# Kernel tuning notes

Measured on AMD Instinct MI355X. Metric: run time of the kernel, lower is better.

## Reference

```python
import jax, jax.numpy as jnp
import numpy as np

BS, S, D, H, DFF, L = 8, 1024, 256, 8, 1024, 3
DK = D // H
NEG = -1e32


def setup_inputs() -> dict:
    key = jax.random.key(0)
    ks = jax.random.split(key, 10)
    r = lambda k, shp: jax.random.normal(k, shp, jnp.float32) * 0.02
    return {
        "q_embed_data": jax.random.normal(ks[0], (BS, S, D), jnp.float32),
        "qa_embed_data": jax.random.normal(ks[1], (BS, S, D), jnp.float32),
        "Wk": r(ks[2], (L, D, D)), "bk": jnp.zeros((L, D), jnp.float32),
        "Wv": r(ks[3], (L, D, D)), "bv": jnp.zeros((L, D), jnp.float32),
        "Wo": r(ks[4], (L, D, D)), "bo": jnp.zeros((L, D), jnp.float32),
        "gammas": r(ks[5], (L, H)),
        "ln1_g": jnp.ones((L, D), jnp.float32), "ln1_b": jnp.zeros((L, D), jnp.float32),
        "W1": r(ks[6], (L, D, DFF)), "b1": jnp.zeros((L, DFF), jnp.float32),
        "W2": r(ks[7], (L, DFF, D)), "b2": jnp.zeros((L, D), jnp.float32),
        "ln2_g": jnp.ones((L, D), jnp.float32), "ln2_b": jnp.zeros((L, D), jnp.float32),
    }


def _layernorm(x, g, b, eps=1e-5):
    mu = x.mean(-1, keepdims=True)
    var = ((x - mu) ** 2).mean(-1, keepdims=True)
    return (x - mu) * jax.lax.rsqrt(var + eps) * g + b


def _attn(xq, xk, xv, Wk, bk, Wv, bv, Wo, bo, gamma, mask, zero_pad):
    # kq_same=1: q and k both use k_linear
    bs = xq.shape[0]
    q = (xq @ Wk + bk).reshape(bs, S, H, DK).transpose(0, 2, 1, 3)  # bhsd
    k = (xk @ Wk + bk).reshape(bs, S, H, DK).transpose(0, 2, 1, 3)
    v = (xv @ Wv + bv).reshape(bs, S, H, DK).transpose(0, 2, 1, 3)
    scores = jnp.einsum('bhid,bhjd->bhij', q, k) / np.float32(np.sqrt(DK))
    mf = mask.astype(scores.dtype)
    # no-grad decay branch (detached in torch)
    p = jax.nn.softmax(jnp.where(mask, scores, NEG), axis=-1) * mf
    distcum = jnp.cumsum(p, axis=-1)
    disttot = p.sum(axis=-1, keepdims=True)
    idx = jnp.arange(S)
    pos = jnp.abs(idx[None, :] - idx[:, None]).astype(jnp.float32)[None, None]
    dist = jnp.sqrt(jnp.clip((disttot - distcum) * pos, 0.0, None))
    dist = jax.lax.stop_gradient(dist)
    g = -jax.nn.softplus(gamma)[None, :, None, None]  # (1,H,1,1)
    total_effect = jnp.clip(jnp.exp(dist * g), 1e-5, 1e5)
    scores = scores * total_effect
    attn = jax.nn.softmax(jnp.where(mask, scores, NEG), axis=-1)
    if zero_pad:
        attn = attn.at[:, :, 0, :].set(0.0)
    out = jnp.einsum('bhij,bhjd->bhid', attn, v)
    out = out.transpose(0, 2, 1, 3).reshape(bs, S, D)
    return out @ Wo + bo


def _block(i, xq, xk, xv, mask, zero_pad, apply_pos, P):
    Wk, bk, Wv, bv, Wo, bo, gam, l1g, l1b, W1, b1, W2, b2, l2g, l2b = [p[i] for p in P]
    q2 = _attn(xq, xk, xv, Wk, bk, Wv, bv, Wo, bo, gam, mask, zero_pad)
    x = _layernorm(xq + q2, l1g, l1b)
    if apply_pos:
        ff = jax.nn.relu(x @ W1 + b1) @ W2 + b2
        x = _layernorm(x + ff, l2g, l2b)
    return x


def _forward(q_embed_data, qa_embed_data, Wk, bk, Wv, bv, Wo, bo, gammas,
             ln1_g, ln1_b, W1, b1, W2, b2, ln2_g, ln2_b):
    P = (Wk, bk, Wv, bv, Wo, bo, gammas, ln1_g, ln1_b, W1, b1, W2, b2, ln2_g, ln2_b)
    tri_incl = jnp.tril(jnp.ones((S, S), bool))[None, None]       # mask=1: peek current+past
    tri_excl = jnp.tril(jnp.ones((S, S), bool), -1)[None, None]   # mask=0: strictly past
    x, y = q_embed_data, qa_embed_data
    # blocks_1 (n_blocks=1): mask=1, apply_pos=True, self-attn on y
    y = _block(0, y, y, y, tri_incl, False, True, P)
    # blocks_2 (2*n_blocks=2): alternate (mask=1, no FFN) / (mask=0, zero_pad, FFN, values=y)
    x = _block(1, x, x, x, tri_incl, False, False, P)
    x = _block(2, x, x, y, tri_excl, True, True, P)
    return x


def reference(q_embed_data, qa_embed_data, Wk, bk, Wv, bv, Wo, bo, gammas,
              ln1_g, ln1_b, W1, b1, W2, b2, ln2_g, ln2_b):
    return _forward(q_embed_data, qa_embed_data, Wk, bk, Wv, bv, Wo, bo, gammas,
                    ln1_g, ln1_b, W1, b1, W2, b2, ln2_g, ln2_b)
```

## Files before the change

kernel.cpp:

```cpp
#include <hip/hip_runtime.h>

typedef unsigned short u16;
typedef float f32x4 __attribute__((ext_vector_type(4)));
typedef __bf16 bf16x8 __attribute__((ext_vector_type(8)));
typedef u16 u16x8 __attribute__((ext_vector_type(8)));
typedef u16 u16x4 __attribute__((ext_vector_type(4)));

__device__ __forceinline__ u16 f2bf(float f) {
  union { float f; unsigned u; } v; v.f = f;
  unsigned r = (v.u + 0x7FFFu + ((v.u >> 16) & 1u)) >> 16;
  return (u16)r;
}
__device__ __forceinline__ unsigned pack2bf(float a, float b) {
  return (unsigned)f2bf(a) | ((unsigned)f2bf(b) << 16);
}
__device__ __forceinline__ float wred_sum(float v) {
#pragma unroll
  for (int o = 32; o >= 1; o >>= 1) v += __shfl_xor(v, o);
  return v;
}

template <int RELU, int WF32, int WBF, int WVT>
__global__ __launch_bounds__(256) void gemm_kernel(
    const u16* __restrict__ A, const u16* __restrict__ Bt,
    const float* __restrict__ bias, float* __restrict__ C,
    u16* __restrict__ Cbf, int M, int N, int K) {
  __shared__ u16 As[64 * 64];
  __shared__ u16 Bs[64 * 64];
  const int tid = threadIdx.x;
  const int lane = tid & 63;
  const int w = tid >> 6;
  const int m0 = blockIdx.x * 64;
  const int n0 = blockIdx.y * 64;
  const int wr = (w >> 1) * 32;
  const int wc = (w & 1) * 32;
  const int l15 = lane & 15, hi = lane >> 4;

  f32x4 acc[2][2] = {};

  for (int k0 = 0; k0 < K; k0 += 64) {
#pragma unroll
    for (int rep = 0; rep < 2; ++rep) {
      int idx = tid + rep * 256;
      int row = idx >> 3, c8 = idx & 7;
      int cs = ((c8 ^ (row & 7)) << 3);
      __builtin_amdgcn_global_load_lds(
          (const __attribute__((address_space(1))) void*)(A + (size_t)(m0 + row) * K + k0 + cs),
          (__attribute__((address_space(3))) void*)(&As[idx * 8]), 16, 0, 0);
      __builtin_amdgcn_global_load_lds(
          (const __attribute__((address_space(1))) void*)(Bt + (size_t)(n0 + row) * K + k0 + cs),
          (__attribute__((address_space(3))) void*)(&Bs[idx * 8]), 16, 0, 0);
    }
    __syncthreads();
#pragma unroll
    for (int kk = 0; kk < 2; ++kk) {
      int kb = (kk * 32 + (hi << 3)) << 1;
      bf16x8 af[2], bfr[2];
#pragma unroll
      for (int mf = 0; mf < 2; ++mf) {
        int m = wr + mf * 16 + l15;
        af[mf] = *(const bf16x8*)((const char*)As + m * 128 + (kb ^ ((m & 7) << 4)));
      }
#pragma unroll
      for (int nf = 0; nf < 2; ++nf) {
        int n = wc + nf * 16 + l15;
        bfr[nf] = *(const bf16x8*)((const char*)Bs + n * 128 + (kb ^ ((n & 7) << 4)));
      }
#pragma unroll
      for (int mf = 0; mf < 2; ++mf)
#pragma unroll
        for (int nf = 0; nf < 2; ++nf)
          acc[mf][nf] = __builtin_amdgcn_mfma_f32_16x16x32_bf16(af[mf], bfr[nf], acc[mf][nf], 0, 0, 0);
    }
    __syncthreads();
  }

#pragma unroll
  for (int mf = 0; mf < 2; ++mf)
#pragma unroll
    for (int nf = 0; nf < 2; ++nf) {
      int col = n0 + wc + nf * 16 + l15;
      float bia = bias[col];
      u16x4 tv;
#pragma unroll
      for (int r = 0; r < 4; ++r) {
        int row = m0 + wr + mf * 16 + (hi << 2) + r;
        float val = acc[mf][nf][r] + bia;
        if (RELU) val = fmaxf(val, 0.f);
        if (WF32) C[(size_t)row * N + col] = val;
        if (WBF) Cbf[(size_t)row * N + col] = f2bf(val);
        if (WVT) tv[r] = f2bf(val);
      }
      if (WVT) {
        int row0 = m0 + wr + mf * 16 + (hi << 2);
        size_t addr = (((size_t)(row0 >> 10) * 8 + (col >> 5)) * 32 + (col & 31)) * 1024 + (row0 & 1023);
        *(u16x4*)(Cbf + addr) = tv;
      }
    }
}

__global__ __launch_bounds__(256) void gemm_kv_kernel(
    const u16* __restrict__ A, const u16* __restrict__ Bt,
    const float* __restrict__ biasK, const float* __restrict__ biasV,
    u16* __restrict__ qkbf, u16* __restrict__ vT, int M, int N, int K) {
  __shared__ u16 As[64 * 64];
  __shared__ u16 Bs[64 * 64];
  const int tid = threadIdx.x;
  const int lane = tid & 63;
  const int w = tid >> 6;
  const int m0 = blockIdx.x * 64;
  const int n0 = blockIdx.y * 64;
  const int wr = (w >> 1) * 32;
  const int wc = (w & 1) * 32;
  const int l15 = lane & 15, hi = lane >> 4;

  f32x4 acc[2][2] = {};

  for (int k0 = 0; k0 < K; k0 += 64) {
#pragma unroll
    for (int rep = 0; rep < 2; ++rep) {
      int idx = tid + rep * 256;
      int row = idx >> 3, c8 = idx & 7;
      int cs = ((c8 ^ (row & 7)) << 3);
      __builtin_amdgcn_global_load_lds(
          (const __attribute__((address_space(1))) void*)(A + (size_t)(m0 + row) * K + k0 + cs),
          (__attribute__((address_space(3))) void*)(&As[idx * 8]), 16, 0, 0);
      __builtin_amdgcn_global_load_lds(
          (const __attribute__((address_space(1))) void*)(Bt + (size_t)(n0 + row) * K + k0 + cs),
          (__attribute__((address_space(3))) void*)(&Bs[idx * 8]), 16, 0, 0);
    }
    __syncthreads();
#pragma unroll
    for (int kk = 0; kk < 2; ++kk) {
      int kb = (kk * 32 + (hi << 3)) << 1;
      bf16x8 af[2], bfr[2];
#pragma unroll
      for (int mf = 0; mf < 2; ++mf) {
        int m = wr + mf * 16 + l15;
        af[mf] = *(const bf16x8*)((const char*)As + m * 128 + (kb ^ ((m & 7) << 4)));
      }
#pragma unroll
      for (int nf = 0; nf < 2; ++nf) {
        int n = wc + nf * 16 + l15;
        bfr[nf] = *(const bf16x8*)((const char*)Bs + n * 128 + (kb ^ ((n & 7) << 4)));
      }
#pragma unroll
      for (int mf = 0; mf < 2; ++mf)
#pragma unroll
        for (int nf = 0; nf < 2; ++nf)
          acc[mf][nf] = __builtin_amdgcn_mfma_f32_16x16x32_bf16(af[mf], bfr[nf], acc[mf][nf], 0, 0, 0);
    }
    __syncthreads();
  }

  const bool isV = (n0 >= 256);
#pragma unroll
  for (int mf = 0; mf < 2; ++mf)
#pragma unroll
    for (int nf = 0; nf < 2; ++nf) {
      int col = n0 + wc + nf * 16 + l15;
      float bia = isV ? biasV[col - 256] : biasK[col];
      u16x4 tv;
#pragma unroll
      for (int r = 0; r < 4; ++r) {
        int row = m0 + wr + mf * 16 + (hi << 2) + r;
        float val = acc[mf][nf][r] + bia;
        if (!isV) qkbf[(size_t)row * 256 + col] = f2bf(val);
        tv[r] = f2bf(val);
      }
      if (isV) {
        int row0 = m0 + wr + mf * 16 + (hi << 2);
        int vc = col - 256;
        size_t addr = (((size_t)(row0 >> 10) * 8 + (vc >> 5)) * 32 + (vc & 31)) * 1024 + (row0 & 1023);
        *(u16x4*)(vT + addr) = tv;
      }
    }
}

__global__ __launch_bounds__(256) void attn_mfma_kernel(
    const u16* __restrict__ qkbf, const u16* __restrict__ vT,
    u16* __restrict__ ao, const float* __restrict__ gam, int excl) {
  __shared__ float zbuf[4][16];
  __shared__ float z2buf[4][16];
  __shared__ float accbuf[8][4][64];

  const int lane = threadIdx.x & 63, w = threadIdx.x >> 6;
  const int qt = 63 - blockIdx.y;
  const int bh = blockIdx.x;
  const int b = bh >> 3, h = bh & 7;
  const int q0 = qt * 16;
  const int l15 = lane & 15, hi = lane >> 4;
  const int i = q0 + l15;
  const float g = -log1pf(__expf(gam[h]));
  const float scale = 0.17677669529663687f;

  const u16* kbase = qkbf + ((size_t)b * 1024) * 256 + h * 32;
  const bf16x8 qfrag = *(const bf16x8*)(kbase + (size_t)(q0 + l15) * 256 + hi * 8);

  const int mylim = i - excl;
  const int jmax = q0 + 15 - excl;
  const int ntiles = (jmax >> 4) + 1;
  const int C = (ntiles + 3) >> 2;
  const int c0 = w * C;
  const int tEnd = (c0 + C < ntiles) ? (c0 + C) : ntiles;
  const int count = (tEnd > c0) ? (tEnd - c0) : 0;

  float zacc = 0.f;
  for (int t = c0; t < tEnd; ++t) {
    bf16x8 kf = *(const bf16x8*)(kbase + (size_t)(t * 16 + l15) * 256 + hi * 8);
    f32x4 sA = {};
    sA = __builtin_amdgcn_mfma_f32_16x16x32_bf16(kf, qfrag, sA, 0, 0, 0);
    const int kb = t * 16 + hi * 4;
#pragma unroll
    for (int r = 0; r < 4; ++r)
      if (kb + r <= mylim) zacc += __expf(sA[r] * scale);
  }
  zacc += __shfl_xor(zacc, 16);
  zacc += __shfl_xor(zacc, 32);
  if (lane < 16) zbuf[w][lane] = zacc;
  __syncthreads();

  const float zc0 = zbuf[0][l15], zc1 = zbuf[1][l15];
  const float zc2 = zbuf[2][l15], zc3 = zbuf[3][l15];
  const float Z = zc0 + zc1 + zc2 + zc3;
  const float invZ = Z > 0.f ? 1.f / Z : 0.f;
  float prefix = 0.f;
  if (w > 0) prefix += zc0;
  if (w > 1) prefix += zc1;
  if (w > 2) prefix += zc2;

  const u16* vbase = vT + (size_t)bh * 32 * 1024;
  float carry = prefix * invZ, z2 = 0.f;
  f32x4 accO0 = {}, accO1 = {};
  unsigned pk00 = 0, pk01 = 0;
  const int Cp = (count + 1) & ~1;
  for (int tl = 0; tl < Cp; ++tl) {
    const int t = c0 + tl;
    const bool tv = tl < count;
    float ep[4] = {0.f, 0.f, 0.f, 0.f};
    if (tv) {
      bf16x8 kf = *(const bf16x8*)(kbase + (size_t)(t * 16 + l15) * 256 + hi * 8);
      f32x4 sA = {};
      sA = __builtin_amdgcn_mfma_f32_16x16x32_bf16(kf, qfrag, sA, 0, 0, 0);
      const int kb = t * 16 + hi * 4;
      float sv[4], p[4];
#pragma unroll
      for (int r = 0; r < 4; ++r) {
        sv[r] = sA[r] * scale;
        p[r] = (kb + r <= mylim) ? __expf(sv[r]) * invZ : 0.f;
      }
      float c1 = p[0] + p[1];
      float c2 = c1 + p[2];
      float c3 = c2 + p[3];
      float vsc = c3;
      float tmp = __shfl_up(vsc, 16); if (hi >= 1) vsc += tmp;
      tmp = __shfl_up(vsc, 32); if (hi >= 2) vsc += tmp;
      const float exg = vsc - c3;
      const float tot = __shfl(vsc, l15 + 48);
      const float cb = carry + exg;
      float cum[4] = {cb + p[0], cb + c1, cb + c2, cb + c3};
      carry += tot;
#pragma unroll
      for (int r = 0; r < 4; ++r) {
        if (kb + r <= mylim) {
          float pos = (float)(i - (kb + r));
          float dist = sqrtf(fmaxf((1.f - cum[r]) * pos, 0.f));
          float te = fmaxf(__expf(dist * g), 1e-5f);
          float e = __expf(sv[r] * te);
          ep[r] = e;
          z2 += e;
        }
      }
    }
    unsigned u0 = pack2bf(ep[0], ep[1]);
    unsigned u1 = pack2bf(ep[2], ep[3]);
    if ((tl & 1) == 0) {
      pk00 = u0; pk01 = u1;
    } else {
      const int srcA = l15 + (((2 * hi) & 3) << 4);
      const int srcB = l15 + (((2 * hi + 1) & 3) << 4);
      unsigned a00 = (unsigned)__shfl((int)pk00, srcA);
      unsigned a01 = (unsigned)__shfl((int)u0,   srcA);
      unsigned a10 = (unsigned)__shfl((int)pk01, srcA);
      unsigned a11 = (unsigned)__shfl((int)u1,   srcA);
      unsigned b00 = (unsigned)__shfl((int)pk00, srcB);
      unsigned b01 = (unsigned)__shfl((int)u0,   srcB);
      unsigned b10 = (unsigned)__shfl((int)pk01, srcB);
      unsigned b11 = (unsigned)__shfl((int)u1,   srcB);
      const bool up = hi >= 2;
      union { unsigned u[4]; bf16x8 v; } pf;
      pf.u[0] = up ? a01 : a00;
      pf.u[1] = up ? a11 : a10;
      pf.u[2] = up ? b01 : b00;
      pf.u[3] = up ? b11 : b10;
      const int jb = (t - 1) * 16;
      bf16x8 vf0 = *(const bf16x8*)(vbase + (size_t)l15 * 1024 + jb + hi * 8);
      bf16x8 vf1 = *(const bf16x8*)(vbase + (size_t)(16 + l15) * 1024 + jb + hi * 8);
      accO0 = __builtin_amdgcn_mfma_f32_16x16x32_bf16(vf0, pf.v, accO0, 0, 0, 0);
      accO1 = __builtin_amdgcn_mfma_f32_16x16x32_bf16(vf1, pf.v, accO1, 0, 0, 0);
    }
  }

  z2 += __shfl_xor(z2, 16);
  z2 += __shfl_xor(z2, 32);
  if (lane < 16) z2buf[w][lane] = z2;
#pragma unroll
  for (int j = 0; j < 4; ++j) {
    accbuf[j][w][lane] = accO0[j];
    accbuf[4 + j][w][lane] = accO1[j];
  }
  __syncthreads();

  if (w == 0) {
    const float z2t = z2buf[0][l15] + z2buf[1][l15] + z2buf[2][l15] + z2buf[3][l15];
    const float inv2 = z2t > 0.f ? 1.f / z2t : 0.f;
    u16* aop = ao + ((size_t)(b * 1024 + i)) * 256 + h * 32;
    u16x4 o0, o1;
#pragma unroll
    for (int j = 0; j < 4; ++j) {
      float s0 = accbuf[j][0][lane] + accbuf[j][1][lane] + accbuf[j][2][lane] + accbuf[j][3][lane];
      float s1 = accbuf[4 + j][0][lane] + accbuf[4 + j][1][lane] + accbuf[4 + j][2][lane] + accbuf[4 + j][3][lane];
      o0[j] = f2bf(s0 * inv2);
      o1[j] = f2bf(s1 * inv2);
    }
    *(u16x4*)(aop + hi * 4) = o0;
    *(u16x4*)(aop + 16 + hi * 4) = o1;
  }
}

__global__ __launch_bounds__(256) void add_ln_kernel(
    const float* __restrict__ res, const float* __restrict__ add,
    const float* __restrict__ g, const float* __restrict__ b,
    float* __restrict__ outf, u16* __restrict__ outb) {
  const int lane = threadIdx.x & 63, wid = threadIdx.x >> 6;
  const size_t row = (size_t)blockIdx.x * 4 + wid;
  const size_t base = row * 256 + lane * 4;
  float4 rv = *(const float4*)(res + base);
  float4 av = *(const float4*)(add + base);
  float x0 = rv.x + av.x, x1 = rv.y + av.y, x2 = rv.z + av.z, x3 = rv.w + av.w;
  float sm = wred_sum(x0 + x1 + x2 + x3);
  float mu = sm * (1.f / 256.f);
  float d0 = x0 - mu, d1 = x1 - mu, d2 = x2 - mu, d3 = x3 - mu;
  float vs = wred_sum(d0 * d0 + d1 * d1 + d2 * d2 + d3 * d3);
  float rs = rsqrtf(vs * (1.f / 256.f) + 1e-5f);
  float4 gv = *(const float4*)(g + lane * 4);
  float4 bv = *(const float4*)(b + lane * 4);
  float o0 = d0 * rs * gv.x + bv.x;
  float o1 = d1 * rs * gv.y + bv.y;
  float o2 = d2 * rs * gv.z + bv.z;
  float o3 = d3 * rs * gv.w + bv.w;
  float4 ov = {o0, o1, o2, o3};
  *(float4*)(outf + base) = ov;
  u16x4 wv; wv[0] = f2bf(o0); wv[1] = f2bf(o1); wv[2] = f2bf(o2); wv[3] = f2bf(o3);
  *(u16x4*)(outb + base) = wv;
}

__global__ __launch_bounds__(256) void cast_bf_kernel(
    const float* __restrict__ in, u16* __restrict__ out) {
  size_t i = ((size_t)blockIdx.x * 256 + threadIdx.x) * 8;
  float4 a = *(const float4*)(in + i);
  float4 c = *(const float4*)(in + i + 4);
  u16x8 o;
  o[0] = f2bf(a.x); o[1] = f2bf(a.y); o[2] = f2bf(a.z); o[3] = f2bf(a.w);
  o[4] = f2bf(c.x); o[5] = f2bf(c.y); o[6] = f2bf(c.z); o[7] = f2bf(c.w);
  *(u16x8*)(out + i) = o;
}

__global__ __launch_bounds__(256) void transpose_cast_kernel(
    const float* __restrict__ W, u16* __restrict__ Wt, int K, int N,
    int dstStride) {
  __shared__ float t[32][33];
  const size_t lo = (size_t)blockIdx.z * K * N;
  const size_t lod = (size_t)blockIdx.z * dstStride;
  int n0 = blockIdx.x * 32, k0 = blockIdx.y * 32;
  int tx = threadIdx.x, ty = threadIdx.y;
#pragma unroll
  for (int r = 0; r < 32; r += 8)
    t[ty + r][tx] = W[lo + (size_t)(k0 + ty + r) * N + n0 + tx];
  __syncthreads();
#pragma unroll
  for (int r = 0; r < 32; r += 8)
    Wt[lod + (size_t)(n0 + ty + r) * K + k0 + tx] = f2bf(t[tx][ty + r]);
}

extern "C" void kernel_launch(void* const* d_in, const int* in_sizes, int n_in,
                              void* d_out, int out_size, void* d_ws,
                              size_t ws_size, hipStream_t stream) {
  const float* q_embed = (const float*)d_in[0];
  const float* qa_embed = (const float*)d_in[1];
  const float* Wk = (const float*)d_in[2];
  const float* bk = (const float*)d_in[3];
  const float* Wv = (const float*)d_in[4];
  const float* bv = (const float*)d_in[5];
  const float* Wo = (const float*)d_in[6];
  const float* bo = (const float*)d_in[7];
  const float* gammas = (const float*)d_in[8];
  const float* ln1_g = (const float*)d_in[9];
  const float* ln1_b = (const float*)d_in[10];
  const float* W1 = (const float*)d_in[11];
  const float* b1 = (const float*)d_in[12];
  const float* W2 = (const float*)d_in[13];
  const float* b2 = (const float*)d_in[14];
  const float* ln2_g = (const float*)d_in[15];
  const float* ln2_b = (const float*)d_in[16];

  const size_t ACT_F32 = (size_t)8192 * 256 * 4;
  const size_t ACT_BF = (size_t)8192 * 256 * 2;
  char* p = (char*)d_ws;
  auto carve = [&](size_t bytes) {
    void* r = (void*)p;
    p += (bytes + 255) & ~(size_t)255;
    return r;
  };
  float* yb = (float*)carve(ACT_F32);
  float* xb = (float*)carve(ACT_F32);
  float* pof = (float*)carve(ACT_F32);
  u16* xbf = (u16*)carve(ACT_BF);
  u16* ybf = (u16*)carve(ACT_BF);
  u16* qkbf = (u16*)carve(ACT_BF);
  u16* vTb = (u16*)carve(ACT_BF);
  u16* aobf = (u16*)carve(ACT_BF);
  u16* hbf = (u16*)carve((size_t)8192 * 1024 * 2);
  u16* Wkvt = (u16*)carve((size_t)3 * 131072 * 2);
  u16* Wot = (u16*)carve((size_t)3 * 65536 * 2);
  u16* W1t = (u16*)carve((size_t)3 * 262144 * 2);
  u16* W2t = (u16*)carve((size_t)3 * 262144 * 2);

  dim3 tb(32, 8);
  transpose_cast_kernel<<<dim3(8, 8, 3), tb, 0, stream>>>(Wk, Wkvt, 256, 256, 131072);
  transpose_cast_kernel<<<dim3(8, 8, 3), tb, 0, stream>>>(Wv, Wkvt + 65536, 256, 256, 131072);
  transpose_cast_kernel<<<dim3(8, 8, 3), tb, 0, stream>>>(Wo, Wot, 256, 256, 65536);
  transpose_cast_kernel<<<dim3(32, 8, 3), tb, 0, stream>>>(W1, W1t, 256, 1024, 262144);
  transpose_cast_kernel<<<dim3(8, 32, 3), tb, 0, stream>>>(W2, W2t, 1024, 256, 262144);
  cast_bf_kernel<<<1024, 256, 0, stream>>>(q_embed, xbf);
  cast_bf_kernel<<<1024, 256, 0, stream>>>(qa_embed, ybf);

  const dim3 gP(128, 4), gF(128, 16), gKV(128, 8);
  const dim3 gA(64, 64);

  gemm_kv_kernel<<<gKV, 256, 0, stream>>>(ybf, Wkvt, bk, bv, qkbf, vTb, 8192, 512, 256);
  attn_mfma_kernel<<<gA, 256, 0, stream>>>(qkbf, vTb, aobf, gammas, 0);
  gemm_kernel<0, 1, 0, 0><<<gP, 256, 0, stream>>>(aobf, Wot, bo, pof, nullptr, 8192, 256, 256);
  add_ln_kernel<<<2048, 256, 0, stream>>>(qa_embed, pof, ln1_g, ln1_b, yb, ybf);
  gemm_kernel<1, 0, 1, 0><<<gF, 256, 0, stream>>>(ybf, W1t, b1, nullptr, hbf, 8192, 1024, 256);
  gemm_kernel<0, 1, 0, 0><<<gP, 256, 0, stream>>>(hbf, W2t, b2, pof, nullptr, 8192, 256, 1024);
  add_ln_kernel<<<2048, 256, 0, stream>>>(yb, pof, ln2_g, ln2_b, yb, ybf);

  gemm_kv_kernel<<<gKV, 256, 0, stream>>>(xbf, Wkvt + 131072, bk + 256, bv + 256, qkbf, vTb, 8192, 512, 256);
  attn_mfma_kernel<<<gA, 256, 0, stream>>>(qkbf, vTb, aobf, gammas + 8, 0);
  gemm_kernel<0, 1, 0, 0><<<gP, 256, 0, stream>>>(aobf, Wot + 65536, bo + 256, pof, nullptr, 8192, 256, 256);
  add_ln_kernel<<<2048, 256, 0, stream>>>(q_embed, pof, ln1_g + 256, ln1_b + 256, xb, xbf);

  gemm_kv_kernel<<<gKV, 256, 0, stream>>>(xbf, Wkvt + 262144, bk + 512, bv + 512, qkbf, vTb, 8192, 512, 256);
  gemm_kernel<0, 0, 0, 1><<<gP, 256, 0, stream>>>(ybf, Wkvt + 262144 + 65536, bv + 512, nullptr, vTb, 8192, 256, 256);
  attn_mfma_kernel<<<gA, 256, 0, stream>>>(qkbf, vTb, aobf, gammas + 16, 1);
  gemm_kernel<0, 1, 0, 0><<<gP, 256, 0, stream>>>(aobf, Wot + 131072, bo + 512, pof, nullptr, 8192, 256, 256);
  add_ln_kernel<<<2048, 256, 0, stream>>>(xb, pof, ln1_g + 512, ln1_b + 512, xb, xbf);
  gemm_kernel<1, 0, 1, 0><<<gF, 256, 0, stream>>>(xbf, W1t + 524288, b1 + 2048, nullptr, hbf, 8192, 1024, 256);
  gemm_kernel<0, 1, 0, 0><<<gP, 256, 0, stream>>>(hbf, W2t + 524288, b2 + 512, pof, nullptr, 8192, 256, 1024);
  add_ln_kernel<<<2048, 256, 0, stream>>>(xb, pof, ln2_g + 512, ln2_b + 512, (float*)d_out, xbf);
}
```

Before: 325.5 us.

## Software-pipeline QK MFMA and drop mask checks off the diagonal in attention

The attention kernel now computes the next tile's QK MFMA one iteration ahead, so score computation overlaps the elementwise decay math. Causal mask checks run only on the diagonal tile, and the cumulative-probability math works on unnormalized exponentials with a single scale by invZ, which removes per-element branching and multiplies. The manual bf16 rounding is replaced with the hardware v_cvt_pk_bf16_f32 instruction, and sqrt uses the fast builtin. The lookahead adds register pressure, and the different rounding and sqrt paths may shift numerics slightly.

```diff
diff --git a/kernel.cpp b/kernel.cpp
--- a/kernel.cpp
+++ b/kernel.cpp
@@ -11,8 +11,10 @@
   unsigned r = (v.u + 0x7FFFu + ((v.u >> 16) & 1u)) >> 16;
   return (u16)r;
 }
-__device__ __forceinline__ unsigned pack2bf(float a, float b) {
-  return (unsigned)f2bf(a) | ((unsigned)f2bf(b) << 16);
+__device__ __forceinline__ unsigned cvtpk_bf16(float lo, float hi) {
+  unsigned r;
+  asm("v_cvt_pk_bf16_f32 %0, %1, %2" : "=v"(r) : "v"(lo), "v"(hi));
+  return r;
 }
 __device__ __forceinline__ float wred_sum(float v) {
 #pragma unroll
@@ -195,7 +197,7 @@
   const float scale = 0.17677669529663687f;
 
   const u16* kbase = qkbf + ((size_t)b * 1024) * 256 + h * 32;
-  const bf16x8 qfrag = *(const bf16x8*)(kbase + (size_t)(q0 + l15) * 256 + hi * 8);
+  const bf16x8 qfrag = *(const bf16x8*)(kbase + (size_t)i * 256 + hi * 8);
 
   const int mylim = i - excl;
   const int jmax = q0 + 15 - excl;
@@ -210,10 +212,15 @@
     bf16x8 kf = *(const bf16x8*)(kbase + (size_t)(t * 16 + l15) * 256 + hi * 8);
     f32x4 sA = {};
     sA = __builtin_amdgcn_mfma_f32_16x16x32_bf16(kf, qfrag, sA, 0, 0, 0);
-    const int kb = t * 16 + hi * 4;
-#pragma unroll
-    for (int r = 0; r < 4; ++r)
-      if (kb + r <= mylim) zacc += __expf(sA[r] * scale);
+    if (t == ntiles - 1) {
+      const int kb = t * 16 + hi * 4;
+#pragma unroll
+      for (int r = 0; r < 4; ++r)
+        zacc += (kb + r <= mylim) ? __expf(sA[r] * scale) : 0.f;
+    } else {
+#pragma unroll
+      for (int r = 0; r < 4; ++r) zacc += __expf(sA[r] * scale);
+    }
   }
   zacc += __shfl_xor(zacc, 16);
   zacc += __shfl_xor(zacc, 32);
@@ -230,50 +237,66 @@
   if (w > 2) prefix += zc2;
 
   const u16* vbase = vT + (size_t)bh * 32 * 1024;
-  float carry = prefix * invZ, z2 = 0.f;
+  float carry = prefix, z2 = 0.f;
   f32x4 accO0 = {}, accO1 = {};
   unsigned pk00 = 0, pk01 = 0;
   const int Cp = (count + 1) & ~1;
+
+  f32x4 sA_cur = {};
+  if (count > 0) {
+    bf16x8 kf = *(const bf16x8*)(kbase + (size_t)(c0 * 16 + l15) * 256 + hi * 8);
+    sA_cur = __builtin_amdgcn_mfma_f32_16x16x32_bf16(kf, qfrag, sA_cur, 0, 0, 0);
+  }
   for (int tl = 0; tl < Cp; ++tl) {
     const int t = c0 + tl;
-    const bool tv = tl < count;
-    float ep[4] = {0.f, 0.f, 0.f, 0.f};
-    if (tv) {
-      bf16x8 kf = *(const bf16x8*)(kbase + (size_t)(t * 16 + l15) * 256 + hi * 8);
-      f32x4 sA = {};
-      sA = __builtin_amdgcn_mfma_f32_16x16x32_bf16(kf, qfrag, sA, 0, 0, 0);
+    f32x4 sA_nxt = {};
+    if (tl + 1 < count) {
+      bf16x8 kf = *(const bf16x8*)(kbase + (size_t)((t + 1) * 16 + l15) * 256 + hi * 8);
+      sA_nxt = __builtin_amdgcn_mfma_f32_16x16x32_bf16(kf, qfrag, sA_nxt, 0, 0, 0);
+    }
+    float ep0 = 0.f, ep1 = 0.f, ep2 = 0.f, ep3 = 0.f;
+    if (tl < count) {
       const int kb = t * 16 + hi * 4;
-      float sv[4], p[4];
-#pragma unroll
-      for (int r = 0; r < 4; ++r) {
-        sv[r] = sA[r] * scale;
-        p[r] = (kb + r <= mylim) ? __expf(sv[r]) * invZ : 0.f;
-      }
-      float c1 = p[0] + p[1];
-      float c2 = c1 + p[2];
-      float c3 = c2 + p[3];
-      float vsc = c3;
+      const bool diag = (t == ntiles - 1);
+      const float sv0 = sA_cur[0] * scale, sv1 = sA_cur[1] * scale;
+      const float sv2 = sA_cur[2] * scale, sv3 = sA_cur[3] * scale;
+      float e0 = __expf(sv0), e1 = __expf(sv1);
+      float e2 = __expf(sv2), e3 = __expf(sv3);
+      bool m0 = true, m1 = true, m2 = true, m3 = true;
+      if (diag) {
+        m0 = (kb + 0 <= mylim); m1 = (kb + 1 <= mylim);
+        m2 = (kb + 2 <= mylim); m3 = (kb + 3 <= mylim);
+        e0 = m0 ? e0 : 0.f; e1 = m1 ? e1 : 0.f;
+        e2 = m2 ? e2 : 0.f; e3 = m3 ? e3 : 0.f;
+      }
+      const float cA = e0 + e1, cB = cA + e2, cC = cB + e3;
+      float vsc = cC;
       float tmp = __shfl_up(vsc, 16); if (hi >= 1) vsc += tmp;
       tmp = __shfl_up(vsc, 32); if (hi >= 2) vsc += tmp;
-      const float exg = vsc - c3;
+      const float exg = vsc - cC;
       const float tot = __shfl(vsc, l15 + 48);
       const float cb = carry + exg;
-      float cum[4] = {cb + p[0], cb + c1, cb + c2, cb + c3};
       carry += tot;
-#pragma unroll
-      for (int r = 0; r < 4; ++r) {
-        if (kb + r <= mylim) {
-          float pos = (float)(i - (kb + r));
-          float dist = sqrtf(fmaxf((1.f - cum[r]) * pos, 0.f));
-          float te = fmaxf(__expf(dist * g), 1e-5f);
-          float e = __expf(sv[r] * te);
-          ep[r] = e;
-          z2 += e;
-        }
-      }
-    }
-    unsigned u0 = pack2bf(ep[0], ep[1]);
-    unsigned u1 = pack2bf(ep[2], ep[3]);
+      const float posb = (float)(i - kb);
+      const float cum0 = cb + e0, cum1 = cb + cA, cum2 = cb + cB, cum3 = cb + cC;
+      const float d20 = fmaxf((Z - cum0) * invZ * posb, 0.f);
+      const float d21 = fmaxf((Z - cum1) * invZ * (posb - 1.f), 0.f);
+      const float d22 = fmaxf((Z - cum2) * invZ * (posb - 2.f), 0.f);
+      const float d23 = fmaxf((Z - cum3) * invZ * (posb - 3.f), 0.f);
+      const float te0 = fmaxf(__expf(__builtin_amdgcn_sqrtf(d20) * g), 1e-5f);
+      const float te1 = fmaxf(__expf(__builtin_amdgcn_sqrtf(d21) * g), 1e-5f);
+      const float te2 = fmaxf(__expf(__builtin_amdgcn_sqrtf(d22) * g), 1e-5f);
+      const float te3 = fmaxf(__expf(__builtin_amdgcn_sqrtf(d23) * g), 1e-5f);
+      ep0 = __expf(sv0 * te0); ep1 = __expf(sv1 * te1);
+      ep2 = __expf(sv2 * te2); ep3 = __expf(sv3 * te3);
+      if (diag) {
+        ep0 = m0 ? ep0 : 0.f; ep1 = m1 ? ep1 : 0.f;
+        ep2 = m2 ? ep2 : 0.f; ep3 = m3 ? ep3 : 0.f;
+      }
+      z2 += (ep0 + ep1) + (ep2 + ep3);
+    }
+    const unsigned u0 = cvtpk_bf16(ep0, ep1);
+    const unsigned u1 = cvtpk_bf16(ep2, ep3);
     if ((tl & 1) == 0) {
       pk00 = u0; pk01 = u1;
     } else {
@@ -299,6 +322,7 @@
       accO0 = __builtin_amdgcn_mfma_f32_16x16x32_bf16(vf0, pf.v, accO0, 0, 0, 0);
       accO1 = __builtin_amdgcn_mfma_f32_16x16x32_bf16(vf1, pf.v, accO1, 0, 0, 0);
     }
+    sA_cur = sA_nxt;
   }
 
   z2 += __shfl_xor(z2, 16);
@@ -315,16 +339,17 @@
     const float z2t = z2buf[0][l15] + z2buf[1][l15] + z2buf[2][l15] + z2buf[3][l15];
     const float inv2 = z2t > 0.f ? 1.f / z2t : 0.f;
     u16* aop = ao + ((size_t)(b * 1024 + i)) * 256 + h * 32;
-    u16x4 o0, o1;
+    float s0[4], s1[4];
 #pragma unroll
     for (int j = 0; j < 4; ++j) {
-      float s0 = accbuf[j][0][lane] + accbuf[j][1][lane] + accbuf[j][2][lane] + accbuf[j][3][lane];
-      float s1 = accbuf[4 + j][0][lane] + accbuf[4 + j][1][lane] + accbuf[4 + j][2][lane] + accbuf[4 + j][3][lane];
-      o0[j] = f2bf(s0 * inv2);
-      o1[j] = f2bf(s1 * inv2);
-    }
-    *(u16x4*)(aop + hi * 4) = o0;
-    *(u16x4*)(aop + 16 + hi * 4) = o1;
+      s0[j] = (accbuf[j][0][lane] + accbuf[j][1][lane] + accbuf[j][2][lane] + accbuf[j][3][lane]) * inv2;
+      s1[j] = (accbuf[4 + j][0][lane] + accbuf[4 + j][1][lane] + accbuf[4 + j][2][lane] + accbuf[4 + j][3][lane]) * inv2;
+    }
+    uint2 o0, o1;
+    o0.x = cvtpk_bf16(s0[0], s0[1]); o0.y = cvtpk_bf16(s0[2], s0[3]);
+    o1.x = cvtpk_bf16(s1[0], s1[1]); o1.y = cvtpk_bf16(s1[2], s1[3]);
+    *(uint2*)(aop + hi * 4) = o0;
+    *(uint2*)(aop + 16 + hi * 4) = o1;
   }
 }
 
```

New measurement: 305.2 us. 6.2% less time.
